# Performance work log

Hardware: AMD Instinct MI355X
Metric: run time of the kernel (lower is better)

The kernel has to match this reference:

```python
import jax, jax.numpy as jnp
import numpy as np

B, S, DIM = 2, 2048, 2048
N_HEADS, N_KV_HEADS = 16, 4
HEAD_DIM = DIM // N_HEADS  # 128
N_REP = N_HEADS // N_KV_HEADS  # 4
ROPE_THETA = 10000.0


def setup_inputs() -> dict:
    key = jax.random.key(0)
    ks = jax.random.split(key, 6)
    x = jax.random.normal(ks[0], (B, S, DIM), dtype=jnp.float32)
    # torch nn.Linear weights are [out_features, in_features]
    sc = 0.02
    wq = jax.random.normal(ks[1], (N_HEADS * HEAD_DIM, DIM), dtype=jnp.float32) * sc
    wk = jax.random.normal(ks[2], (N_KV_HEADS * HEAD_DIM, DIM), dtype=jnp.float32) * sc
    wv = jax.random.normal(ks[3], (N_KV_HEADS * HEAD_DIM, DIM), dtype=jnp.float32) * sc
    wo = jax.random.normal(ks[4], (DIM, N_HEADS * HEAD_DIM), dtype=jnp.float32) * sc
    # precomputed rotary table (freqs_cis in llama): [S, head_dim//2]
    inv_freq = 1.0 / (ROPE_THETA ** (jnp.arange(0, HEAD_DIM, 2, dtype=jnp.float32) / HEAD_DIM))
    t = jnp.arange(S, dtype=jnp.float32)
    freqs = jnp.outer(t, inv_freq)  # [S, head_dim//2]
    freqs_cos = jnp.cos(freqs)
    freqs_sin = jnp.sin(freqs)
    # additive causal mask as passed to SDPA (float, 0 on allowed, -inf-like elsewhere)
    causal = jnp.tril(jnp.ones((S, S), dtype=bool))
    mask = jnp.where(causal, 0.0, -1e9).astype(jnp.float32)
    return {"x": x, "wq": wq, "wk": wk, "wv": wv, "wo": wo,
            "freqs_cos": freqs_cos, "freqs_sin": freqs_sin, "mask": mask}


def _apply_rope(t, cos, sin):
    # t: [B, S, H, D]; cos/sin: [S, D//2] -> complex multiply on adjacent pairs
    tr = t.reshape(*t.shape[:-1], -1, 2)  # [B,S,H,D/2,2]
    tre, tim = tr[..., 0], tr[..., 1]
    c = cos[None, :, None, :]
    s = sin[None, :, None, :]
    out_re = tre * c - tim * s
    out_im = tre * s + tim * c
    return jnp.stack([out_re, out_im], axis=-1).reshape(t.shape)


def reference(x, wq, wk, wv, wo, freqs_cos, freqs_sin, mask):
    Bx, Sx, _ = x.shape
    xq = (x @ wq.T).reshape(Bx, Sx, N_HEADS, HEAD_DIM)
    xk = (x @ wk.T).reshape(Bx, Sx, N_KV_HEADS, HEAD_DIM)
    xv = (x @ wv.T).reshape(Bx, Sx, N_KV_HEADS, HEAD_DIM)
    xq = _apply_rope(xq, freqs_cos, freqs_sin)
    xk = _apply_rope(xk, freqs_cos, freqs_sin)
    # repeat_kv for GQA: [B,S,KV,D] -> [B,S,KV*n_rep,D]
    keys = jnp.repeat(xk, N_REP, axis=2)
    values = jnp.repeat(xv, N_REP, axis=2)
    q = xq.transpose(0, 2, 1, 3)      # [B,H,S,D]
    k = keys.transpose(0, 2, 1, 3)
    v = values.transpose(0, 2, 1, 3)
    scale = 1.0 / jnp.sqrt(jnp.float32(HEAD_DIM))
    scores = jnp.einsum('bhqd,bhkd->bhqk', q, k) * scale + mask[None, None]
    attn = jax.nn.softmax(scores, axis=-1)
    out = jnp.einsum('bhqk,bhkd->bhqd', attn, v)
    out = out.transpose(0, 2, 1, 3).reshape(Bx, Sx, -1)
    return out @ wo.T
```

## Files before the change

### kernel.cpp

```cpp
#include <hip/hip_runtime.h>
#include <hip/hip_bf16.h>

#define B_   2
#define S_   2048
#define DIM_ 2048
#define NH   16
#define NKV  4
#define HD   128
#define QKVN 3072

typedef __attribute__((ext_vector_type(8)))  short  sv8;
typedef __attribute__((ext_vector_type(8)))  ushort usv8;
typedef __attribute__((ext_vector_type(4)))  float  fv4;
typedef __attribute__((ext_vector_type(16))) float  fv16;

__device__ __forceinline__ float fast_exp2(float x) {
  return __builtin_amdgcn_exp2f(x);
}

__device__ __forceinline__ ushort f2bf(float f) {
  __hip_bfloat16 h = __float2bfloat16(f);
  union { __hip_bfloat16 h; ushort u; } c; c.h = h; return c.u;
}
__device__ __forceinline__ float bf2f(ushort u) {
  union { unsigned int i; float f; } c; c.i = ((unsigned)u) << 16; return c.f;
}

__device__ __forceinline__ unsigned int cvtpk(float lo, float hi) {
  unsigned int r;
  asm("v_cvt_pk_bf16_f32 %0, %1, %2" : "=v"(r) : "v"(lo), "v"(hi));
  return r;
}
__device__ __forceinline__ unsigned int xhalf(unsigned int x) {
  return (unsigned int)__shfl_xor((int)x, 32, 64);
}

__device__ __forceinline__ float tmax16(const fv16& v) {
  float a = fmaxf(fmaxf(v[0], v[1]),  fmaxf(v[2], v[3]));
  float b = fmaxf(fmaxf(v[4], v[5]),  fmaxf(v[6], v[7]));
  float c = fmaxf(fmaxf(v[8], v[9]),  fmaxf(v[10], v[11]));
  float d = fmaxf(fmaxf(v[12], v[13]), fmaxf(v[14], v[15]));
  return fmaxf(fmaxf(a, b), fmaxf(c, d));
}
__device__ __forceinline__ float tsum16(const fv16& v) {
  float a = (v[0] + v[1]) + (v[2] + v[3]);
  float b = (v[4] + v[5]) + (v[6] + v[7]);
  float c = (v[8] + v[9]) + (v[10] + v[11]);
  float d = (v[12] + v[13]) + (v[14] + v[15]);
  return (a + b) + (c + d);
}

__device__ __forceinline__ void async16(const void* g, void* l) {
  __builtin_amdgcn_global_load_lds(
      (const __attribute__((address_space(1))) unsigned int*)g,
      (__attribute__((address_space(3))) unsigned int*)l, 16, 0, 0);
}

__global__ void cvt_kernel(const float* __restrict__ in, ushort* __restrict__ out, int n) {
  int i = (blockIdx.x * 256 + threadIdx.x) * 4;
  if (i >= n) return;
  fv4 v = *(const fv4*)(in + i);
  ushort4 o;
  o.x = f2bf(v[0]); o.y = f2bf(v[1]); o.z = f2bf(v[2]); o.w = f2bf(v[3]);
  *(ushort4*)(out + i) = o;
}

__global__ void rope_kernel(const ushort* __restrict__ raw, const float* __restrict__ fc,
                            const float* __restrict__ fs, ushort* __restrict__ out,
                            int heads, int rowstride, float scale) {
  int t = blockIdx.x * 256 + threadIdx.x;
  int grp = t & 15;
  int h   = (t >> 4) % heads;
  int s   = ((t >> 4) / heads) % S_;
  int b   = t / (16 * heads * S_);
  const ushort* src = raw + (size_t)(b * S_ + s) * rowstride + h * HD + grp * 8;
  sv8 v = *(const sv8*)src;
  fv4 c  = *(const fv4*)(fc + s * 64 + grp * 4);
  fv4 sn = *(const fv4*)(fs + s * 64 + grp * 4);
  sv8 o;
#pragma unroll
  for (int p = 0; p < 4; ++p) {
    float re = bf2f((ushort)v[2 * p]);
    float im = bf2f((ushort)v[2 * p + 1]);
    float orr = (re * c[p] - im * sn[p]) * scale;
    float oi  = (re * sn[p] + im * c[p]) * scale;
    o[2 * p]     = (short)f2bf(orr);
    o[2 * p + 1] = (short)f2bf(oi);
  }
  ushort* dst = out + ((size_t)(b * heads + h) * S_ + s) * HD + grp * 8;
  *(sv8*)dst = o;
}

__global__ __launch_bounds__(256) void vtrans_kernel(const ushort* __restrict__ vraw,
                                                     ushort* __restrict__ vt, int rowstride) {
  __shared__ ushort tile[128][136];
  int blk = blockIdx.x;
  int st  = blk & 15;
  int kvb = blk >> 4;
  int kv  = kvb & 3;
  int b   = kvb >> 2;
  int s0  = st << 7;
#pragma unroll
  for (int it = 0; it < 8; ++it) {
    int t = it * 256 + threadIdx.x;
    int srow = t >> 4;
    int d8 = (t & 15) * 8;
    usv8 v = *(const usv8*)(vraw + (size_t)(b * S_ + s0 + srow) * rowstride + kv * HD + d8);
#pragma unroll
    for (int j = 0; j < 8; ++j) tile[d8 + j][srow] = v[j];
  }
  __syncthreads();
#pragma unroll
  for (int it = 0; it < 8; ++it) {
    int t = it * 256 + threadIdx.x;
    int d = t >> 4;
    int s8 = (t & 15) * 8;
    usv8 o;
#pragma unroll
    for (int j = 0; j < 8; ++j) o[j] = tile[d][s8 + j];
    *(usv8*)(vt + ((size_t)(b * NKV + kv) * HD + d) * S_ + s0 + s8) = o;
  }
}

template <typename OutT>
__global__ __launch_bounds__(256) void gemm_bt(const ushort* __restrict__ A,
                                               const ushort* __restrict__ Bm,
                                               OutT* __restrict__ C,
                                               int M, int N, int K) {
  __shared__ ushort As[128 * 64];
  __shared__ ushort Bs[128 * 64];
  int nb = N >> 7;
  int bx = blockIdx.x % nb;
  int by = blockIdx.x / nb;
  int m0 = by << 7, n0 = bx << 7;
  int lane = threadIdx.x & 63, w = threadIdx.x >> 6;
  int l15 = lane & 15, lg = lane >> 4;
  int wm = (w >> 1) * 64, wn = (w & 1) * 64;

  const ushort* aSrc[4]; const ushort* bSrc[4];
  ushort* aDst[4]; ushort* bDst[4];
#pragma unroll
  for (int it = 0; it < 4; ++it) {
    int lin = it * 4096 + w * 1024 + lane * 16;
    int row = lin >> 7;
    int cb  = (lin & 127) ^ ((row & 7) << 4);
    aSrc[it] = A  + (size_t)(m0 + row) * K + (cb >> 1);
    bSrc[it] = Bm + (size_t)(n0 + row) * K + (cb >> 1);
    aDst[it] = As + ((it * 4096 + w * 1024) >> 1);
    bDst[it] = Bs + ((it * 4096 + w * 1024) >> 1);
  }

  fv4 acc[4][4] = {};

  for (int kt = 0; kt < K; kt += 64) {
#pragma unroll
    for (int it = 0; it < 4; ++it) async16(aSrc[it] + kt, aDst[it]);
#pragma unroll
    for (int it = 0; it < 4; ++it) async16(bSrc[it] + kt, bDst[it]);
    __syncthreads();
#pragma unroll
    for (int kk = 0; kk < 2; ++kk) {
      sv8 af[4], bfr[4];
#pragma unroll
      for (int i = 0; i < 4; ++i) {
        int row = wm + i * 16 + l15;
        int byt = row * 128 + ((kk * 64 + (lg << 4)) ^ ((row & 7) << 4));
        af[i] = *(const sv8*)((const char*)As + byt);
      }
#pragma unroll
      for (int j = 0; j < 4; ++j) {
        int row = wn + j * 16 + l15;
        int byt = row * 128 + ((kk * 64 + (lg << 4)) ^ ((row & 7) << 4));
        bfr[j] = *(const sv8*)((const char*)Bs + byt);
      }
#pragma unroll
      for (int i = 0; i < 4; ++i)
#pragma unroll
        for (int j = 0; j < 4; ++j)
          acc[i][j] = __builtin_amdgcn_mfma_f32_16x16x32_bf16(af[i], bfr[j], acc[i][j], 0, 0, 0);
    }
    __syncthreads();
  }

#pragma unroll
  for (int i = 0; i < 4; ++i)
#pragma unroll
    for (int j = 0; j < 4; ++j)
#pragma unroll
      for (int r = 0; r < 4; ++r) {
        int row = m0 + wm + i * 16 + (lg << 2) + r;
        int col = n0 + wn + j * 16 + l15;
        if constexpr (sizeof(OutT) == 2) C[(size_t)row * N + col] = (OutT)f2bf(acc[i][j][r]);
        else                             C[(size_t)row * N + col] = (OutT)acc[i][j][r];
      }
}

__global__ __launch_bounds__(256, 2) void attn_kernel(const ushort* __restrict__ Q,
                                                      const ushort* __restrict__ Kr,
                                                      const ushort* __restrict__ Vt,
                                                      ushort* __restrict__ O) {
  __shared__ ushort Ks[2][64 * 128];
  __shared__ ushort Vs[2][128 * 64];

  int blk = blockIdx.x;
  int bh  = blk & 31;
  int pr  = blk >> 5;
  int h   = bh & 15;
  int b   = bh >> 4;
  int kv  = h >> 2;
  int lane = threadIdx.x & 63, w = threadIdx.x >> 6;
  int l31 = lane & 31, hh = lane >> 5;

  const ushort* Qbase = Q  + (size_t)(b * NH  + h ) * S_ * HD;
  const ushort* Kbase = Kr + (size_t)(b * NKV + kv) * S_ * HD;
  const ushort* Vbase = Vt + (size_t)(b * NKV + kv) * HD * S_;

  const ushort* kSrc[4]; ushort* kDst[4];
  const ushort* vSrc[4]; ushort* vDst[4];
#pragma unroll
  for (int it = 0; it < 4; ++it) {
    int lin = it * 4096 + w * 1024 + lane * 16;
    { int row = lin >> 8; int cb = (lin & 255) ^ ((row & 7) << 4);
      kSrc[it] = Kbase + (size_t)row * HD + (cb >> 1);
      kDst[it] = Ks[0] + ((it * 4096 + w * 1024) >> 1); }
    { int row = lin >> 7; int cb = (lin & 127) ^ ((row & 7) << 4);
      vSrc[it] = Vbase + (size_t)row * S_ + (cb >> 1);
      vDst[it] = Vs[0] + ((it * 4096 + w * 1024) >> 1); }
  }

  for (int pass = 0; pass < 2; ++pass) {
    int qt = pass ? (15 - pr) : pr;
    int q0 = qt << 7;
    int qrow_w = q0 + w * 32;
    int myq    = qrow_w + l31;

    sv8 qf[8];
#pragma unroll
    for (int kk = 0; kk < 8; ++kk)
      qf[kk] = *(const sv8*)(Qbase + (size_t)myq * HD + kk * 16 + hh * 8);

    fv16 oacc[4] = {};
    float mrun = -1e30f, lrun = 0.f;

    int nkt = (q0 >> 6) + 2;

    if (pass) __syncthreads();

#pragma unroll
    for (int it = 0; it < 4; ++it) async16(kSrc[it], kDst[it]);
#pragma unroll
    for (int it = 0; it < 4; ++it) async16(vSrc[it], vDst[it]);

    for (int kt = 0; kt < nkt; ++kt) {
      int cur = kt & 1, nxt = cur ^ 1;
      __syncthreads();
      if (kt + 1 < nkt) {
        size_t k0n = (size_t)(kt + 1) << 6;
#pragma unroll
        for (int it = 0; it < 4; ++it) async16(kSrc[it] + k0n * HD, kDst[it] + nxt * (64 * 128));
#pragma unroll
        for (int it = 0; it < 4; ++it) async16(vSrc[it] + k0n,      vDst[it] + nxt * (128 * 64));
      }
      const char* KsC = (const char*)Ks[cur];
      const char* VsC = (const char*)Vs[cur];
      int k0 = kt << 6;

      fv16 sacc[2] = {};
      __builtin_amdgcn_s_setprio(1);
#pragma unroll
      for (int kk = 0; kk < 8; ++kk) {
        int cb = kk * 32 + hh * 16;
        int r0 = l31, r1 = 32 + l31;
        sv8 kf0 = *(const sv8*)(KsC + r0 * 256 + (cb ^ ((r0 & 7) << 4)));
        sv8 kf1 = *(const sv8*)(KsC + r1 * 256 + (cb ^ ((r1 & 7) << 4)));
        sacc[0] = __builtin_amdgcn_mfma_f32_32x32x16_bf16(kf0, qf[kk], sacc[0], 0, 0, 0);
        sacc[1] = __builtin_amdgcn_mfma_f32_32x32x16_bf16(kf1, qf[kk], sacc[1], 0, 0, 0);
      }
      __builtin_amdgcn_s_setprio(0);

      if (k0 + 63 > qrow_w) {
        int thr = myq - k0 - 4 * hh;
#pragma unroll
        for (int t = 0; t < 2; ++t)
#pragma unroll
          for (int r = 0; r < 16; ++r) {
            int kp = t * 32 + (r & 3) + 8 * (r >> 2);
            if (kp > thr) sacc[t][r] = -1e30f;
          }
      }

      float tmax = fmaxf(tmax16(sacc[0]), tmax16(sacc[1]));
      tmax = fmaxf(tmax, __shfl_xor(tmax, 32, 64));

      if (__any(tmax > mrun + 8.0f)) {
        float mnew = fmaxf(mrun, tmax);
        float esc  = fast_exp2(mrun - mnew);
        lrun *= esc;
        float er[16];
#pragma unroll
        for (int r = 0; r < 16; ++r) er[r] = __shfl(esc, (r & 3) + 8 * (r >> 2) + 4 * hh, 64);
#pragma unroll
        for (int d0 = 0; d0 < 4; ++d0)
#pragma unroll
          for (int r = 0; r < 16; ++r) oacc[d0][r] *= er[r];
        mrun = mnew;
      }

#pragma unroll
      for (int t = 0; t < 2; ++t)
#pragma unroll
        for (int r = 0; r < 16; ++r) sacc[t][r] = fast_exp2(sacc[t][r] - mrun);
      float psum = tsum16(sacc[0]) + tsum16(sacc[1]);
      psum += __shfl_xor(psum, 32, 64);
      lrun += psum;

      union Frag { unsigned int u[4]; sv8 v; } pa[4];
#pragma unroll
      for (int t = 0; t < 2; ++t)
#pragma unroll
        for (int half = 0; half < 2; ++half) {
          int cb = half * 8;
          unsigned int a0 = cvtpk(sacc[t][cb + 0], sacc[t][cb + 1]);
          unsigned int a1 = cvtpk(sacc[t][cb + 2], sacc[t][cb + 3]);
          unsigned int b0 = cvtpk(sacc[t][cb + 4], sacc[t][cb + 5]);
          unsigned int b1 = cvtpk(sacc[t][cb + 6], sacc[t][cb + 7]);
          unsigned int a0p = xhalf(a0), a1p = xhalf(a1);
          unsigned int b0p = xhalf(b0), b1p = xhalf(b1);
          pa[2 * t + half].u[0] = hh ? b0p : a0;
          pa[2 * t + half].u[1] = hh ? b1p : a1;
          pa[2 * t + half].u[2] = hh ? b0  : a0p;
          pa[2 * t + half].u[3] = hh ? b1  : a1p;
        }

      __builtin_amdgcn_s_setprio(1);
#pragma unroll
      for (int ks = 0; ks < 4; ++ks) {
        int cb = ks * 32 + hh * 16;
#pragma unroll
        for (int d0 = 0; d0 < 4; ++d0) {
          int row = d0 * 32 + l31;
          sv8 vf = *(const sv8*)(VsC + row * 128 + (cb ^ ((row & 7) << 4)));
          oacc[d0] = __builtin_amdgcn_mfma_f32_32x32x16_bf16(pa[ks].v, vf, oacc[d0], 0, 0, 0);
        }
      }
      __builtin_amdgcn_s_setprio(0);
    }

    float inv = 1.0f / lrun;
    float ir[16];
#pragma unroll
    for (int r = 0; r < 16; ++r) ir[r] = __shfl(inv, (r & 3) + 8 * (r >> 2) + 4 * hh, 64);
#pragma unroll
    for (int r = 0; r < 16; ++r) {
      int q = qrow_w + (r & 3) + 8 * (r >> 2) + 4 * hh;
#pragma unroll
      for (int d0 = 0; d0 < 4; ++d0) {
        int d = d0 * 32 + l31;
        O[(size_t)(b * S_ + q) * DIM_ + h * HD + d] = f2bf(oacc[d0][r] * ir[r]);
      }
    }
  }
}

extern "C" void kernel_launch(void* const* d_in, const int* in_sizes, int n_in,
                              void* d_out, int out_size, void* d_ws, size_t ws_size,
                              hipStream_t stream) {
  const float* x  = (const float*)d_in[0];
  const float* wq = (const float*)d_in[1];
  const float* wk = (const float*)d_in[2];
  const float* wv = (const float*)d_in[3];
  const float* wo = (const float*)d_in[4];
  const float* fc = (const float*)d_in[5];
  const float* fs = (const float*)d_in[6];
  float* out = (float*)d_out;

  char* ws = (char*)d_ws;
  size_t off = 0;
  auto alloc = [&](size_t bytes) -> ushort* {
    ushort* p = (ushort*)(ws + off);
    off += (bytes + 255) & ~(size_t)255;
    return p;
  };
  ushort* xb    = alloc((size_t)B_ * S_ * DIM_ * 2);
  ushort* wqkvb = alloc((size_t)QKVN * DIM_ * 2);
  ushort* wob   = alloc((size_t)DIM_ * DIM_ * 2);
  ushort* qkvr  = alloc((size_t)B_ * S_ * QKVN * 2);
  ushort* qr    = alloc((size_t)B_ * S_ * DIM_ * 2);
  ushort* kr    = alloc((size_t)B_ * S_ * NKV * HD * 2);
  ushort* vtb   = alloc((size_t)B_ * S_ * NKV * HD * 2);
  ushort* obf   = alloc((size_t)B_ * S_ * DIM_ * 2);
  (void)ws_size; (void)n_in; (void)in_sizes; (void)out_size;

  cvt_kernel<<<(B_ * S_ * DIM_) / 1024, 256, 0, stream>>>(x,  xb, B_ * S_ * DIM_);
  cvt_kernel<<<(DIM_ * DIM_) / 1024,     256, 0, stream>>>(wq, wqkvb,                 DIM_ * DIM_);
  cvt_kernel<<<(NKV * HD * DIM_) / 1024, 256, 0, stream>>>(wk, wqkvb + 2048 * DIM_,   NKV * HD * DIM_);
  cvt_kernel<<<(NKV * HD * DIM_) / 1024, 256, 0, stream>>>(wv, wqkvb + 2560 * DIM_,   NKV * HD * DIM_);
  cvt_kernel<<<(DIM_ * DIM_) / 1024,     256, 0, stream>>>(wo, wob, DIM_ * DIM_);

  gemm_bt<ushort><<<(B_ * S_ / 128) * (QKVN / 128), 256, 0, stream>>>(xb, wqkvb, qkvr,
                                                                     B_ * S_, QKVN, DIM_);

  const float qscale = 0.08838834764831845f * 1.4426950408889634f;
  rope_kernel<<<(B_ * S_ * NH  * 16) / 256, 256, 0, stream>>>(qkvr,        fc, fs, qr, NH,  QKVN, qscale);
  rope_kernel<<<(B_ * S_ * NKV * 16) / 256, 256, 0, stream>>>(qkvr + 2048, fc, fs, kr, NKV, QKVN, 1.0f);
  vtrans_kernel<<<B_ * NKV * (S_ / 128), 256, 0, stream>>>(qkvr + 2560, vtb, QKVN);

  attn_kernel<<<B_ * NH * 8, 256, 0, stream>>>(qr, kr, vtb, obf);

  gemm_bt<float><<<(B_ * S_ / 128) * (DIM_ / 128), 256, 0, stream>>>(obf, wob, out, B_ * S_, DIM_, DIM_);
}
```

Measured before the change: 216.7 us.

## Split attention KV range across two warp halves and merge partial softmax

Doubles the attention block to 512 threads. The two groups of four waves each process half of the causal KV tiles for the same 128 query rows, each with its own double-buffered K/V shared memory. The partial max, sum and output accumulators are then merged through shared memory before the store. This is meant to halve the serial KV loop length per block and raise parallelism, given there are only 256 blocks. The cost is 128KB of LDS per block, which limits blocks per CU, plus extra syncs and a merge step.

```diff
diff --git a/kernel.cpp b/kernel.cpp
--- a/kernel.cpp
+++ b/kernel.cpp
@@ -195,12 +195,11 @@
       }
 }
 
-__global__ __launch_bounds__(256, 2) void attn_kernel(const ushort* __restrict__ Q,
+__global__ __launch_bounds__(512, 2) void attn_kernel(const ushort* __restrict__ Q,
                                                       const ushort* __restrict__ Kr,
                                                       const ushort* __restrict__ Vt,
                                                       ushort* __restrict__ O) {
-  __shared__ ushort Ks[2][64 * 128];
-  __shared__ ushort Vs[2][128 * 64];
+  __shared__ __align__(16) ushort SMEM[65536];
 
   int blk = blockIdx.x;
   int bh  = blk & 31;
@@ -209,30 +208,39 @@
   int b   = bh >> 4;
   int kv  = h >> 2;
   int lane = threadIdx.x & 63, w = threadIdx.x >> 6;
+  int wg = w & 3, Hf = w >> 2;
   int l31 = lane & 31, hh = lane >> 5;
 
   const ushort* Qbase = Q  + (size_t)(b * NH  + h ) * S_ * HD;
   const ushort* Kbase = Kr + (size_t)(b * NKV + kv) * S_ * HD;
   const ushort* Vbase = Vt + (size_t)(b * NKV + kv) * HD * S_;
 
-  const ushort* kSrc[4]; ushort* kDst[4];
-  const ushort* vSrc[4]; ushort* vDst[4];
+  const ushort* kSrc[4]; ushort* kDst[2][4];
+  const ushort* vSrc[4]; ushort* vDst[2][4];
 #pragma unroll
   for (int it = 0; it < 4; ++it) {
-    int lin = it * 4096 + w * 1024 + lane * 16;
+    int lin = it * 4096 + wg * 1024 + lane * 16;
     { int row = lin >> 8; int cb = (lin & 255) ^ ((row & 7) << 4);
-      kSrc[it] = Kbase + (size_t)row * HD + (cb >> 1);
-      kDst[it] = Ks[0] + ((it * 4096 + w * 1024) >> 1); }
+      kSrc[it] = Kbase + (size_t)row * HD + (cb >> 1); }
     { int row = lin >> 7; int cb = (lin & 127) ^ ((row & 7) << 4);
-      vSrc[it] = Vbase + (size_t)row * S_ + (cb >> 1);
-      vDst[it] = Vs[0] + ((it * 4096 + w * 1024) >> 1); }
-  }
+      vSrc[it] = Vbase + (size_t)row * S_ + (cb >> 1); }
+#pragma unroll
+    for (int buf = 0; buf < 2; ++buf) {
+      kDst[buf][it] = SMEM + Hf * 16384 + buf * 8192 + ((it * 4096 + wg * 1024) >> 1);
+      vDst[buf][it] = SMEM + 32768 + Hf * 16384 + buf * 8192 + ((it * 4096 + wg * 1024) >> 1);
+    }
+  }
+
+  float* cML = (float*)SMEM;
+  float* cO  = (float*)SMEM + 512;
 
   for (int pass = 0; pass < 2; ++pass) {
     int qt = pass ? (15 - pr) : pr;
     int q0 = qt << 7;
-    int qrow_w = q0 + w * 32;
+    int qrow_w = q0 + wg * 32;
     int myq    = qrow_w + l31;
+    int nj     = qt + 1;
+    int ktbase = Hf * nj;
 
     sv8 qf[8];
 #pragma unroll
@@ -242,28 +250,27 @@
     fv16 oacc[4] = {};
     float mrun = -1e30f, lrun = 0.f;
 
-    int nkt = (q0 >> 6) + 2;
-
-    if (pass) __syncthreads();
-
-#pragma unroll
-    for (int it = 0; it < 4; ++it) async16(kSrc[it], kDst[it]);
-#pragma unroll
-    for (int it = 0; it < 4; ++it) async16(vSrc[it], vDst[it]);
-
-    for (int kt = 0; kt < nkt; ++kt) {
-      int cur = kt & 1, nxt = cur ^ 1;
+    {
+      size_t k0 = (size_t)ktbase << 6;
+#pragma unroll
+      for (int it = 0; it < 4; ++it) async16(kSrc[it] + k0 * HD, kDst[0][it]);
+#pragma unroll
+      for (int it = 0; it < 4; ++it) async16(vSrc[it] + k0,      vDst[0][it]);
+    }
+
+    for (int j = 0; j < nj; ++j) {
+      int cur = j & 1, nxt = cur ^ 1;
       __syncthreads();
-      if (kt + 1 < nkt) {
-        size_t k0n = (size_t)(kt + 1) << 6;
-#pragma unroll
-        for (int it = 0; it < 4; ++it) async16(kSrc[it] + k0n * HD, kDst[it] + nxt * (64 * 128));
-#pragma unroll
-        for (int it = 0; it < 4; ++it) async16(vSrc[it] + k0n,      vDst[it] + nxt * (128 * 64));
-      }
-      const char* KsC = (const char*)Ks[cur];
-      const char* VsC = (const char*)Vs[cur];
-      int k0 = kt << 6;
+      if (j + 1 < nj) {
+        size_t k0n = (size_t)(ktbase + j + 1) << 6;
+#pragma unroll
+        for (int it = 0; it < 4; ++it) async16(kSrc[it] + k0n * HD, kDst[nxt][it]);
+#pragma unroll
+        for (int it = 0; it < 4; ++it) async16(vSrc[it] + k0n,      vDst[nxt][it]);
+      }
+      const char* KsC = (const char*)(SMEM + Hf * 16384 + cur * 8192);
+      const char* VsC = (const char*)(SMEM + 32768 + Hf * 16384 + cur * 8192);
+      int k0 = (ktbase + j) << 6;
 
       fv16 sacc[2] = {};
       __builtin_amdgcn_s_setprio(1);
@@ -285,7 +292,7 @@
 #pragma unroll
           for (int r = 0; r < 16; ++r) {
             int kp = t * 32 + (r & 3) + 8 * (r >> 2);
-            if (kp > thr) sacc[t][r] = -1e30f;
+            if (kp > thr) sacc[t][r] = -1e38f;
           }
       }
 
@@ -346,19 +353,46 @@
       __builtin_amdgcn_s_setprio(0);
     }
 
-    float inv = 1.0f / lrun;
-    float ir[16];
-#pragma unroll
-    for (int r = 0; r < 16; ++r) ir[r] = __shfl(inv, (r & 3) + 8 * (r >> 2) + 4 * hh, 64);
-#pragma unroll
-    for (int r = 0; r < 16; ++r) {
-      int q = qrow_w + (r & 3) + 8 * (r >> 2) + 4 * hh;
-#pragma unroll
-      for (int d0 = 0; d0 < 4; ++d0) {
-        int d = d0 * 32 + l31;
-        O[(size_t)(b * S_ + q) * DIM_ + h * HD + d] = f2bf(oacc[d0][r] * ir[r]);
-      }
-    }
+    __syncthreads();
+    if (Hf) {
+      int base = wg * 64 + lane;
+      cML[base * 2]     = mrun;
+      cML[base * 2 + 1] = lrun;
+      float* dst = cO + base * 65;
+#pragma unroll
+      for (int d0 = 0; d0 < 4; ++d0)
+#pragma unroll
+        for (int r = 0; r < 16; ++r) dst[d0 * 16 + r] = oacc[d0][r];
+    }
+    __syncthreads();
+    if (!Hf) {
+      int base = wg * 64 + lane;
+      float m2 = cML[base * 2], l2 = cML[base * 2 + 1];
+      const float* src = cO + base * 65;
+      float m  = fmaxf(mrun, m2);
+      float e1 = fast_exp2(mrun - m), e2 = fast_exp2(m2 - m);
+      float l  = lrun * e1 + l2 * e2;
+      float inv = 1.0f / l;
+      float f1 = e1 * inv, f2 = e2 * inv;
+      float f1b[16], f2b[16];
+#pragma unroll
+      for (int r = 0; r < 16; ++r) {
+        int ro = (r & 3) + 8 * (r >> 2) + 4 * hh;
+        f1b[r] = __shfl(f1, ro, 64);
+        f2b[r] = __shfl(f2, ro, 64);
+      }
+#pragma unroll
+      for (int r = 0; r < 16; ++r) {
+        int q = qrow_w + (r & 3) + 8 * (r >> 2) + 4 * hh;
+#pragma unroll
+        for (int d0 = 0; d0 < 4; ++d0) {
+          int d = d0 * 32 + l31;
+          float val = oacc[d0][r] * f1b[r] + src[d0 * 16 + r] * f2b[r];
+          O[(size_t)(b * S_ + q) * DIM_ + h * HD + d] = f2bf(val);
+        }
+      }
+    }
+    __syncthreads();
   }
 }
 
@@ -405,7 +439,7 @@
   rope_kernel<<<(B_ * S_ * NKV * 16) / 256, 256, 0, stream>>>(qkvr + 2048, fc, fs, kr, NKV, QKVN, 1.0f);
   vtrans_kernel<<<B_ * NKV * (S_ / 128), 256, 0, stream>>>(qkvr + 2560, vtb, QKVN);
 
-  attn_kernel<<<B_ * NH * 8, 256, 0, stream>>>(qr, kr, vtb, obf);
+  attn_kernel<<<B_ * NH * 8, 512, 0, stream>>>(qr, kr, vtb, obf);
 
   gemm_bt<float><<<(B_ * S_ / 128) * (DIM_ / 128), 256, 0, stream>>>(obf, wob, out, B_ * S_, DIM_, DIM_);
 }
```

After: 201.5 us. 7.0% less time.
